# Optimization experiments

Measured on AMD Instinct MI355X. Metric: run time of the kernel, lower is better.

Reference implementation:

```python
import jax, jax.numpy as jnp
import numpy as np

L_DEG = 4      # max out-degree L
DEPTH = 7      # complete L-ary tree depth -> 21845 nodes
N_GEN = 16
C_ST = 8
M_LAB = 256


def _build_tree():
    sizes = [L_DEG ** d for d in range(DEPTH + 1)]
    limits = np.concatenate([[0], np.cumsum(sizes)]).astype(np.int64)
    t_size = int(limits[-1])
    nodes = np.arange(t_size)
    rng = np.random.default_rng(0)
    labels = rng.integers(0, M_LAB, t_size)
    parent = np.where(nodes > 0, (nodes - 1) // L_DEG, 0)
    pos = np.where(nodes > 0, (nodes - 1) % L_DEG, 0)
    ch = np.zeros((t_size, L_DEG), dtype=np.int64)
    n_internal = int(limits[-2])
    ch[:n_internal] = L_DEG * nodes[:n_internal, None] + np.arange(1, L_DEG + 1)[None, :]
    t = np.concatenate([labels[:, None], parent[:, None], pos[:, None], ch], axis=1).astype(np.int64)
    return t, limits


def setup_inputs() -> dict:
    key = jax.random.key(0)
    ka, kb, kp, ks = jax.random.split(key, 4)
    t, limits = _build_tree()
    return {
        "t": jnp.asarray(t),
        "t_limits": jnp.asarray(limits),
        "a": jax.random.normal(ka, (N_GEN, C_ST, C_ST, L_DEG), dtype=jnp.float32),
        "b": jax.random.normal(kb, (N_GEN, C_ST, M_LAB), dtype=jnp.float32),
        "pi": jax.random.normal(kp, (N_GEN, C_ST, L_DEG), dtype=jnp.float32),
        "sp": jax.random.normal(ks, (N_GEN, L_DEG), dtype=jnp.float32),
    }


def _forward(tn, lim, a, b, pi, sp):
    # tn, lim are host numpy int arrays (tree structure is a constant).
    G, C, _, L = a.shape
    t_size = int(lim[-1])
    n_levels = len(lim) - 1
    sL = int(lim[-2])                      # first leaf index
    labels = tn[:, 0]
    posf = tn[:, 2]
    ch_all = tn[:, 3:3 + L]

    sm_a = jax.nn.softmax(a, axis=1)       # P(parent_state i | child_state j, pos l)
    sm_b = jax.nn.softmax(b, axis=2)
    sm_pi = jax.nn.softmax(pi, axis=1)
    sm_sp = jax.nn.softmax(sp, axis=1)
    a_sp = sm_a * sm_sp[:, None, None, :]  # [G,i,j,L]

    # ---------------- upward pass ----------------
    prior = jnp.zeros((t_size, G, C), a.dtype)
    beta = jnp.zeros((t_size, G, C), a.dtype)
    beta_il = jnp.zeros((t_size, G, C), a.dtype)

    prior_lv = jnp.moveaxis(sm_pi[:, :, posf[sL:]], 2, 0)   # [NL,G,C]
    emis_lv = jnp.moveaxis(sm_b[:, :, labels[sL:]], 2, 0)   # [NL,G,C]
    beta_lv = prior_lv * emis_lv
    beta_lv = beta_lv / jnp.sum(beta_lv, axis=2, keepdims=True)
    prior = prior.at[sL:].set(prior_lv)
    beta = beta.at[sL:].set(beta_lv)

    for lev in range(n_levels - 2, -1, -1):   # internal levels, bottom-up
        s, e = int(lim[lev]), int(lim[lev + 1])
        ch = ch_all[s:e]                       # [P,L]
        mask = (ch > 0).astype(a.dtype)        # children packed in first slots
        prior_ch = prior[ch]                   # [P,L,G,C]
        beta_ch = beta[ch]                     # [P,L,G,C]
        u_prior = jnp.einsum('gijl,pl,plgj->pgi', a_sp, mask, prior_ch)
        u_bil = jnp.einsum('gijl,pl,plgj->pgi', a_sp, mask, beta_ch) / u_prior
        emis = jnp.moveaxis(sm_b[:, :, labels[s:e]], 2, 0)  # [P,G,C]
        tmp = emis * u_bil * u_prior
        u_beta = tmp / jnp.sum(tmp, axis=2, keepdims=True)
        prior = prior.at[s:e].set(u_prior)
        beta = beta.at[s:e].set(u_beta)
        beta_il = beta_il.at[s:e].set(u_bil)

    # ---------------- downward pass ----------------
    # row t_size is a dummy slot for padded (absent) children
    eps_i = jnp.zeros((t_size + 1, G, C), a.dtype).at[0].set(beta[0])
    eps_ijl = jnp.zeros((t_size, G, C, C, L), a.dtype)
    for lev in range(0, n_levels - 1):         # parents, top-down (root included)
        s, e = int(lim[lev]), int(lim[lev + 1])
        ch = ch_all[s:e]
        maskb = ch > 0
        mask = maskb.astype(a.dtype)
        beta_ch = jnp.transpose(beta[ch], (0, 2, 3, 1))       # [P,G,Cj,L]
        pe = eps_i[s:e] / (prior[s:e] * beta_il[s:e])         # [P,G,Ci]
        res = (pe[:, :, :, None, None] * a_sp[None]
               * beta_ch[:, :, None, :, :]
               * mask[:, None, None, None, :])                # [P,G,i,j,L]
        child_eps = jnp.sum(res, axis=3)                       # sum over j (as in source) -> [P,G,i,L]
        vals = jnp.moveaxis(child_eps, 3, 1).reshape(-1, G, C) # [P*L,G,C]
        safe = np.where(maskb, ch, t_size).reshape(-1)
        eps_i = eps_i.at[safe].set(vals)
        eps_ijl = eps_ijl.at[s:e].set(res)
    eps_i = eps_i[:t_size]
    # leaves' eps_ijl stay zero (source scatters zeros there)

    # ---------------- log-likelihood ----------------
    a_lh = jnp.einsum('ugijl,gijl->g', eps_ijl, jnp.log(sm_a))
    b_lh = jnp.einsum('ugc,gcu->g', eps_i, jnp.log(sm_b)[:, :, labels])
    pi_lh = jnp.einsum('ugc,gcu->g', eps_i[sL:], jnp.log(sm_pi)[:, :, posf[sL:]])
    eps_l = jnp.sum(eps_ijl, axis=(2, 3))                      # [u,g,L]
    sp_lh = jnp.einsum('ugl,gl->g', eps_l, jnp.log(sm_sp))
    return a_lh + b_lh + pi_lh + sp_lh


def reference(t, t_limits, a, b, pi, sp):
    tn = np.asarray(t)
    lim = np.asarray(t_limits)
    return _forward(tn, lim, a, b, pi, sp)
```

## Files before the change

### kernel.cpp

```cpp
#include <hip/hip_runtime.h>


#define G 16
#define C 8
#define GC 128
#define TSIZE 21845
#define SL 5461

__device__ __forceinline__ float grp8_sum(float v) {
  v += __shfl_xor(v, 1);
  v += __shfl_xor(v, 2);
  v += __shfl_xor(v, 4);
  return v;
}

__global__ void setup_kernel(const float* __restrict__ ain, const float* __restrict__ bin,
                             const float* __restrict__ piin, const float* __restrict__ spin,
                             float* __restrict__ a_sp, float* __restrict__ log_a,
                             float* __restrict__ sm_bT, float* __restrict__ log_bT,
                             float* __restrict__ sm_piT, float* __restrict__ log_piT,
                             float* __restrict__ log_sp, unsigned* __restrict__ ctr) {
  int blk = blockIdx.x, tid = threadIdx.x;
  if (blk < 128) {
    __shared__ float red4[4];
    int row = blk;
    float x = bin[row * 256 + tid];
    float m = x;
    #pragma unroll
    for (int off2 = 32; off2; off2 >>= 1) m = fmaxf(m, __shfl_xor(m, off2));
    if ((tid & 63) == 0) red4[tid >> 6] = m;
    __syncthreads();
    m = fmaxf(fmaxf(red4[0], red4[1]), fmaxf(red4[2], red4[3]));
    __syncthreads();
    float e = expf(x - m);
    float ssum = e;
    #pragma unroll
    for (int off2 = 32; off2; off2 >>= 1) ssum += __shfl_xor(ssum, off2);
    if ((tid & 63) == 0) red4[tid >> 6] = ssum;
    __syncthreads();
    ssum = red4[0] + red4[1] + red4[2] + red4[3];
    sm_bT[tid * GC + row]  = e / ssum;
    log_bT[tid * GC + row] = (x - m) - logf(ssum);
  } else if (blk == 128) {
    for (int col = tid; col < 512; col += 256) {
      int g = col >> 5, j = (col >> 2) & 7, l = col & 3;
      float x[8], m = -1e30f;
      #pragma unroll
      for (int i = 0; i < 8; ++i) { x[i] = ain[g*256 + i*32 + j*4 + l]; m = fmaxf(m, x[i]); }
      float ssum = 0.f;
      #pragma unroll
      for (int i = 0; i < 8; ++i) ssum += expf(x[i] - m);
      float ls = logf(ssum);
      float y0 = spin[g*4+0], y1 = spin[g*4+1], y2 = spin[g*4+2], y3 = spin[g*4+3];
      float ms = fmaxf(fmaxf(y0, y1), fmaxf(y2, y3));
      float d = expf(y0-ms) + expf(y1-ms) + expf(y2-ms) + expf(y3-ms);
      float spv = expf(spin[g*4+l] - ms) / d;
      #pragma unroll
      for (int i = 0; i < 8; ++i) {
        int o2 = g*256 + i*32 + j*4 + l;
        float smv = expf(x[i] - m) / ssum;
        a_sp[o2]  = smv * spv;
        log_a[o2] = (x[i] - m) - ls;
      }
    }
  } else {
    if (tid < 64) {
      int g = tid >> 2, l = tid & 3;
      float x[8], m = -1e30f;
      #pragma unroll
      for (int c = 0; c < 8; ++c) { x[c] = piin[g*32 + c*4 + l]; m = fmaxf(m, x[c]); }
      float ssum = 0.f;
      #pragma unroll
      for (int c = 0; c < 8; ++c) ssum += expf(x[c] - m);
      float ls = logf(ssum);
      #pragma unroll
      for (int c = 0; c < 8; ++c) {
        sm_piT[l*GC + g*8 + c]  = expf(x[c] - m) / ssum;
        log_piT[l*GC + g*8 + c] = (x[c] - m) - ls;
      }
    } else if (tid < 80) {
      int g = tid - 64;
      float y[4], m = -1e30f;
      #pragma unroll
      for (int l = 0; l < 4; ++l) { y[l] = spin[g*4 + l]; m = fmaxf(m, y[l]); }
      float ssum = 0.f;
      #pragma unroll
      for (int l = 0; l < 4; ++l) ssum += expf(y[l] - m);
      float ls = logf(ssum);
      #pragma unroll
      for (int l = 0; l < 4; ++l) log_sp[g*4 + l] = (y[l] - m) - ls;
    } else if (tid == 80) {
      *ctr = 0u;
    }
  }
}

__device__ __forceinline__ void up_lds(int v, int lab, int gi, int g8,
    const float* asp, const float* __restrict__ sm_bT,
    float* sBeta, float* sNum, bool wantNum) {
  int ch0 = 4*v + 1;
  float ub = 0.f;
  #pragma unroll
  for (int l = 0; l < 4; ++l) {
    const float4* bp = (const float4*)(sBeta + (ch0 + l)*GC + g8);
    float4 b0 = bp[0], b1 = bp[1];
    ub += asp[l]*b0.x + asp[4+l]*b0.y + asp[8+l]*b0.z + asp[12+l]*b0.w
        + asp[16+l]*b1.x + asp[20+l]*b1.y + asp[24+l]*b1.z + asp[28+l]*b1.w;
  }
  float tmp = sm_bT[lab*GC + gi] * ub;
  float s = grp8_sum(tmp);
  sBeta[v*GC + gi] = tmp / s;
  if (wantNum) sNum[v*GC + gi] = ub;
}

__device__ __forceinline__ double down_lds(int v, int lab, float e, int gi, int g8,
    const float* asp, const float* aal, const float* lsp,
    const float* __restrict__ log_bT, float* sBeta, const float* sNum) {
  float pe = e / sNum[v*GC + gi];
  int ch0 = 4*v + 1;
  float local = 0.f;
  #pragma unroll
  for (int l = 0; l < 4; ++l) {
    float4* bp = (float4*)(sBeta + (ch0 + l)*GC + g8);
    float4 b0 = bp[0], b1 = bp[1];
    float S = asp[l]*b0.x + asp[4+l]*b0.y + asp[8+l]*b0.z + asp[12+l]*b0.w
            + asp[16+l]*b1.x + asp[20+l]*b1.y + asp[24+l]*b1.z + asp[28+l]*b1.w;
    float A = aal[l]*b0.x + aal[4+l]*b0.y + aal[8+l]*b0.z + aal[12+l]*b0.w
            + aal[16+l]*b1.x + aal[20+l]*b1.y + aal[24+l]*b1.z + aal[28+l]*b1.w;
    float ce = pe * S;
    sBeta[(ch0 + l)*GC + gi] = ce;
    local += pe*A + ce*lsp[l];
  }
  return (double)local + (double)(e * log_bT[lab*GC + gi]);
}

__global__ __launch_bounds__(512, 1) void up_kernel(
    const float* __restrict__ a_sp, const float* __restrict__ sm_bT,
    const float* __restrict__ sm_piT, const int* __restrict__ t,
    float* __restrict__ betaS, float* __restrict__ numS) {
  __shared__ float sBeta[85*GC];
  __shared__ float sNum[21*GC];
  const int blk = blockIdx.x, tid = threadIdx.x;
  const int gi = tid & 127, g = gi >> 3, i = gi & 7, g8 = g*8, w = tid >> 7;
  float asp[32];
  {
    const float4* pa = (const float4*)(a_sp + g*256 + i*32);
    #pragma unroll
    for (int q = 0; q < 8; ++q) {
      float4 v = pa[q];
      asp[q*4+0]=v.x; asp[q*4+1]=v.y; asp[q*4+2]=v.z; asp[q*4+3]=v.w;
    }
  }
  const int base_leaf = SL + blk*64;
  #pragma unroll
  for (int it = 0; it < 16; ++it) {
    int k = it*4 + w;
    float bt = sm_piT[(k & 3)*GC + gi] * sm_bT[t[(base_leaf + k)*7]*GC + gi];
    float s = grp8_sum(bt);
    sBeta[(21 + k)*GC + gi] = bt / s;
  }
  __syncthreads();
  #pragma unroll
  for (int it = 0; it < 4; ++it) {
    int k = it*4 + w;
    up_lds(5 + k, t[(1365 + blk*16 + k)*7], gi, g8, asp, sm_bT, sBeta, sNum, true);
  }
  __syncthreads();
  up_lds(1 + w, t[(341 + blk*4 + w)*7], gi, g8, asp, sm_bT, sBeta, sNum, true);
  __syncthreads();
  if (tid < 128)
    up_lds(0, t[(85 + blk)*7], gi, g8, asp, sm_bT, sBeta, sNum, true);
  __syncthreads();
  {
    const float4* srcB = (const float4*)sBeta;
    float4* dstB = (float4*)(betaS + (size_t)blk*85*GC);
    for (int n = tid; n < 85*GC/4; n += 512) dstB[n] = srcB[n];
    const float4* srcN = (const float4*)sNum;
    float4* dstN = (float4*)(numS + (size_t)blk*21*GC);
    for (int n = tid; n < 21*GC/4; n += 512) dstN[n] = srcN[n];
  }
}

__global__ __launch_bounds__(512, 1) void downall_kernel(
    const float* __restrict__ a_sp, const float* __restrict__ log_a,
    const float* __restrict__ log_sp, const float* __restrict__ sm_bT,
    const float* __restrict__ log_bT, const float* __restrict__ sm_piT,
    const float* __restrict__ log_piT, const int* __restrict__ t,
    const float* __restrict__ betaS, const float* __restrict__ numS,
    unsigned* __restrict__ ctr, double* __restrict__ partial,
    float* __restrict__ out) {
  __shared__ float  sBeta[85*GC];
  __shared__ float  sNum[21*GC];
  __shared__ float  sEps[GC];
  __shared__ double sd[64];
  __shared__ double sfin[256];
  __shared__ unsigned lastFlag;
  const int blk = blockIdx.x, tid = threadIdx.x;
  const int gi = tid & 127, g = gi >> 3, i = gi & 7, g8 = g*8, w = tid >> 7;
  float asp[32], aal[32], lsp[4];
  {
    const float4* pa = (const float4*)(a_sp  + g*256 + i*32);
    const float4* pl = (const float4*)(log_a + g*256 + i*32);
    #pragma unroll
    for (int k = 0; k < 8; ++k) {
      float4 va = pa[k], vl = pl[k];
      asp[k*4+0]=va.x; asp[k*4+1]=va.y; asp[k*4+2]=va.z; asp[k*4+3]=va.w;
      aal[k*4+0]=va.x*vl.x; aal[k*4+1]=va.y*vl.y; aal[k*4+2]=va.z*vl.z; aal[k*4+3]=va.w*vl.w;
    }
    #pragma unroll
    for (int l = 0; l < 4; ++l) lsp[l] = log_sp[g*4 + l];
  }

  #pragma unroll
  for (int it = 0; it < 16; ++it) {
    int k = it*4 + w, u = 21 + k;
    float ub = 0.f;
    #pragma unroll
    for (int l = 0; l < 4; ++l) {
      const float4* bp = (const float4*)(betaS + (size_t)(4*k + l)*85*GC + g8);
      float4 b0 = bp[0], b1 = bp[1];
      ub += asp[l]*b0.x + asp[4+l]*b0.y + asp[8+l]*b0.z + asp[12+l]*b0.w
          + asp[16+l]*b1.x + asp[20+l]*b1.y + asp[24+l]*b1.z + asp[28+l]*b1.w;
    }
    float tmp = sm_bT[t[u*7]*GC + gi] * ub;
    float s = grp8_sum(tmp);
    sBeta[u*GC + gi] = tmp / s;
  }
  __syncthreads();
  #pragma unroll
  for (int it = 0; it < 4; ++it) {
    int u = 5 + it*4 + w;
    up_lds(u, t[u*7], gi, g8, asp, sm_bT, sBeta, sNum, true);
  }
  __syncthreads();
  up_lds(1 + w, t[(1 + w)*7], gi, g8, asp, sm_bT, sBeta, sNum, true);
  __syncthreads();
  if (tid < 128)
    up_lds(0, t[0], gi, g8, asp, sm_bT, sBeta, sNum, true);
  __syncthreads();

  double acc = 0.0;
  if (tid < 128) {
    int a1 = 1 + (blk >> 6), a2 = 5 + (blk >> 4), a3 = 21 + (blk >> 2);
    float e = sBeta[gi];
    int anc[3] = {0, a1, a2};
    int chn[3] = {a1, a2, a3};
    #pragma unroll
    for (int s2 = 0; s2 < 3; ++s2) {
      float pe = e / sNum[anc[s2]*GC + gi];
      int l = (chn[s2] - 1) & 3;
      const float4* bp = (const float4*)(sBeta + chn[s2]*GC + g8);
      float4 b0 = bp[0], b1 = bp[1];
      float S = asp[l]*b0.x + asp[4+l]*b0.y + asp[8+l]*b0.z + asp[12+l]*b0.w
              + asp[16+l]*b1.x + asp[20+l]*b1.y + asp[24+l]*b1.z + asp[28+l]*b1.w;
      e = pe * S;
    }
    float Sv[4], Av[4], num3 = 0.f;
    int qbase = blk & ~3;
    #pragma unroll
    for (int l = 0; l < 4; ++l) {
      const float4* bp = (const float4*)(betaS + (size_t)(qbase + l)*85*GC + g8);
      float4 b0 = bp[0], b1 = bp[1];
      Sv[l] = asp[l]*b0.x + asp[4+l]*b0.y + asp[8+l]*b0.z + asp[12+l]*b0.w
            + asp[16+l]*b1.x + asp[20+l]*b1.y + asp[24+l]*b1.z + asp[28+l]*b1.w;
      num3 += Sv[l];
      Av[l] = aal[l]*b0.x + aal[4+l]*b0.y + aal[8+l]*b0.z + aal[12+l]*b0.w
            + aal[16+l]*b1.x + aal[20+l]*b1.y + aal[24+l]*b1.z + aal[28+l]*b1.w;
    }
    float e3 = e;
    float pe3 = e3 / num3;
    sEps[gi] = pe3 * Sv[blk & 3];
    if ((blk & 3) == 0) {
      float local = 0.f;
      #pragma unroll
      for (int l = 0; l < 4; ++l) local += pe3*Av[l] + (pe3*Sv[l])*lsp[l];
      acc += (double)local + (double)(e3 * log_bT[t[a3*7]*GC + gi]);
    }
  }
  __syncthreads();

  if (blk == 0) {
    if (tid < 128)
      acc += down_lds(0, t[0], sBeta[gi], gi, g8, asp, aal, lsp, log_bT, sBeta, sNum);
    __syncthreads();
    {
      int v = 1 + w;
      acc += down_lds(v, t[v*7], sBeta[v*GC + gi], gi, g8, asp, aal, lsp, log_bT, sBeta, sNum);
    }
    __syncthreads();
    #pragma unroll
    for (int it = 0; it < 4; ++it) {
      int v = 5 + it*4 + w;
      acc += down_lds(v, t[v*7], sBeta[v*GC + gi], gi, g8, asp, aal, lsp, log_bT, sBeta, sNum);
    }
    __syncthreads();
  }

  {
    const float4* srcB = (const float4*)(betaS + (size_t)blk*85*GC);
    float4* dstB = (float4*)sBeta;
    for (int n = tid; n < 85*GC/4; n += 512) dstB[n] = srcB[n];
    const float4* srcN = (const float4*)(numS + (size_t)blk*21*GC);
    float4* dstN = (float4*)sNum;
    for (int n = tid; n < 21*GC/4; n += 512) dstN[n] = srcN[n];
  }
  __syncthreads();

  const int base_leaf = SL + blk*64;
  if (tid < 128)
    acc += down_lds(0, t[(85 + blk)*7], sEps[gi], gi, g8, asp, aal, lsp,
                    log_bT, sBeta, sNum);
  __syncthreads();
  {
    int v = 1 + w;
    acc += down_lds(v, t[(341 + blk*4 + w)*7], sBeta[v*GC + gi], gi, g8,
                    asp, aal, lsp, log_bT, sBeta, sNum);
  }
  __syncthreads();
  #pragma unroll
  for (int it = 0; it < 4; ++it) {
    int k = it*4 + w, v = 5 + k;
    acc += down_lds(v, t[(1365 + blk*16 + k)*7], sBeta[v*GC + gi], gi, g8,
                    asp, aal, lsp, log_bT, sBeta, sNum);
  }
  __syncthreads();
  #pragma unroll
  for (int it = 0; it < 16; ++it) {
    int k = it*4 + w;
    float e = sBeta[(21 + k)*GC + gi];
    acc += (double)(e * (log_bT[t[(base_leaf + k)*7]*GC + gi] +
                         log_piT[(k & 3)*GC + gi]));
  }

  acc += __shfl_xor(acc, 1);
  acc += __shfl_xor(acc, 2);
  acc += __shfl_xor(acc, 4);
  if (i == 0) sd[tid >> 3] = acc;
  __syncthreads();
  if (tid < 16) partial[blk*16 + tid] = sd[tid] + sd[16 + tid] + sd[32 + tid] + sd[48 + tid];
  __syncthreads();

  if (tid == 0) {
    unsigned old = __hip_atomic_fetch_add(ctr, 1u, __ATOMIC_ACQ_REL,
                                          __HIP_MEMORY_SCOPE_AGENT);
    lastFlag = (old == 255u);
  }
  __syncthreads();
  if (lastFlag) {
    if (tid < 256) {
      int gg = tid & 15, ch = tid >> 4;
      const double* p = partial + (size_t)ch*256 + gg;
      double s = 0.0;
      #pragma unroll
      for (int q = 0; q < 16; ++q) s += p[q*16];
      sfin[tid] = s;
    }
    __syncthreads();
    if (tid < 16) {
      double tot = 0.0;
      #pragma unroll
      for (int ch = 0; ch < 16; ++ch) tot += sfin[ch*16 + tid];
      out[tid] = (float)tot;
    }
  }
}

extern "C" void kernel_launch(void* const* d_in, const int* in_sizes, int n_in,
                              void* d_out, int out_size, void* d_ws, size_t ws_size,
                              hipStream_t stream) {
  const int*   t  = (const int*)d_in[0];
  const float* a  = (const float*)d_in[2];
  const float* b  = (const float*)d_in[3];
  const float* pi = (const float*)d_in[4];
  const float* sp = (const float*)d_in[5];
  float* out = (float*)d_out;

  char* w = (char*)d_ws;
  size_t off = 0;
  auto carve = [&](size_t bytes) -> void* {
    void* ptr = w + off;
    off += (bytes + 255) & ~(size_t)255;
    return ptr;
  };
  float*    a_sp    = (float*)carve((size_t)16*8*8*4*4);
  float*    log_a   = (float*)carve((size_t)16*8*8*4*4);
  float*    sm_bT   = (float*)carve((size_t)256*GC*4);
  float*    log_bT  = (float*)carve((size_t)256*GC*4);
  float*    sm_piT  = (float*)carve((size_t)4*GC*4);
  float*    log_piT = (float*)carve((size_t)4*GC*4);
  float*    log_sp  = (float*)carve((size_t)16*4*4);
  float*    betaS   = (float*)carve((size_t)256*85*GC*4);
  float*    numS    = (float*)carve((size_t)256*21*GC*4);
  double*   partial = (double*)carve((size_t)256*16*8);
  unsigned* ctr     = (unsigned*)carve((size_t)4);

  setup_kernel<<<130, 256, 0, stream>>>(a, b, pi, sp, a_sp, log_a, sm_bT, log_bT,
                                        sm_piT, log_piT, log_sp, ctr);
  up_kernel<<<256, 512, 0, stream>>>(a_sp, sm_bT, sm_piT, t, betaS, numS);
  downall_kernel<<<256, 512, 0, stream>>>(a_sp, log_a, log_sp, sm_bT, log_bT,
                                          sm_piT, log_piT, t, betaS, numS,
                                          ctr, partial, out);
}
```

Measured before the change: 107.1 us.

## Prefetch subtree state into registers and spread top-level downward pass across blocks

The up kernel now writes each subtree root's beta to a compact betaG array, so the downall kernel reads top-level betas from a small contiguous buffer instead of strided rows in betaS. The downall kernel issues its per-block betaS/numS loads into registers at kernel start, which lets them overlap the redundant top-of-tree computation, and stores them to LDS later. The serial top-three-level downward pass that block 0 used to run alone is split so each of blocks 0-20 handles one node, recomputing its ancestor eps chain. This trades higher register pressure and some redundant arithmetic for less serialization and hidden load latency.

Result: no change. 105.6 us (-1.4%).

```diff
diff --git a/kernel.cpp b/kernel.cpp
--- a/kernel.cpp
+++ b/kernel.cpp
@@ -12,6 +12,13 @@
   v += __shfl_xor(v, 2);
   v += __shfl_xor(v, 4);
   return v;
+}
+
+__device__ __forceinline__ float matv(const float* asp, const float* row, int l, int g8) {
+  const float4* bp = (const float4*)(row + g8);
+  float4 b0 = bp[0], b1 = bp[1];
+  return asp[l]*b0.x + asp[4+l]*b0.y + asp[8+l]*b0.z + asp[12+l]*b0.w
+       + asp[16+l]*b1.x + asp[20+l]*b1.y + asp[24+l]*b1.z + asp[28+l]*b1.w;
 }
 
 __global__ void setup_kernel(const float* __restrict__ ain, const float* __restrict__ bin,
@@ -137,7 +144,8 @@
 __global__ __launch_bounds__(512, 1) void up_kernel(
     const float* __restrict__ a_sp, const float* __restrict__ sm_bT,
     const float* __restrict__ sm_piT, const int* __restrict__ t,
-    float* __restrict__ betaS, float* __restrict__ numS) {
+    float* __restrict__ betaS, float* __restrict__ numS,
+    float* __restrict__ betaG) {
   __shared__ float sBeta[85*GC];
   __shared__ float sNum[21*GC];
   const int blk = blockIdx.x, tid = threadIdx.x;
@@ -168,8 +176,10 @@
   __syncthreads();
   up_lds(1 + w, t[(341 + blk*4 + w)*7], gi, g8, asp, sm_bT, sBeta, sNum, true);
   __syncthreads();
-  if (tid < 128)
+  if (tid < 128) {
     up_lds(0, t[(85 + blk)*7], gi, g8, asp, sm_bT, sBeta, sNum, true);
+    betaG[(size_t)blk*GC + gi] = sBeta[gi];
+  }
   __syncthreads();
   {
     const float4* srcB = (const float4*)sBeta;
@@ -187,8 +197,8 @@
     const float* __restrict__ log_bT, const float* __restrict__ sm_piT,
     const float* __restrict__ log_piT, const int* __restrict__ t,
     const float* __restrict__ betaS, const float* __restrict__ numS,
-    unsigned* __restrict__ ctr, double* __restrict__ partial,
-    float* __restrict__ out) {
+    const float* __restrict__ betaG, unsigned* __restrict__ ctr,
+    double* __restrict__ partial, float* __restrict__ out) {
   __shared__ float  sBeta[85*GC];
   __shared__ float  sNum[21*GC];
   __shared__ float  sEps[GC];
@@ -211,17 +221,25 @@
     for (int l = 0; l < 4; ++l) lsp[l] = log_sp[g*4 + l];
   }
 
+  float4 rB0, rB1, rB2, rB3, rB4, rB5, rN0, rN1;
+  {
+    const float4* srcB = (const float4*)(betaS + (size_t)blk*85*GC);
+    rB0 = srcB[tid];        rB1 = srcB[tid + 512];
+    rB2 = srcB[tid + 1024]; rB3 = srcB[tid + 1536];
+    rB4 = srcB[tid + 2048];
+    if (tid < 160) rB5 = srcB[tid + 2560];
+    const float4* srcN = (const float4*)(numS + (size_t)blk*21*GC);
+    rN0 = srcN[tid];
+    if (tid < 160) rN1 = srcN[tid + 512];
+  }
+
   #pragma unroll
   for (int it = 0; it < 16; ++it) {
     int k = it*4 + w, u = 21 + k;
     float ub = 0.f;
     #pragma unroll
-    for (int l = 0; l < 4; ++l) {
-      const float4* bp = (const float4*)(betaS + (size_t)(4*k + l)*85*GC + g8);
-      float4 b0 = bp[0], b1 = bp[1];
-      ub += asp[l]*b0.x + asp[4+l]*b0.y + asp[8+l]*b0.z + asp[12+l]*b0.w
-          + asp[16+l]*b1.x + asp[20+l]*b1.y + asp[24+l]*b1.z + asp[28+l]*b1.w;
-    }
+    for (int l = 0; l < 4; ++l)
+      ub += matv(asp, betaG + (size_t)(4*k + l)*GC, l, g8);
     float tmp = sm_bT[t[u*7]*GC + gi] * ub;
     float s = grp8_sum(tmp);
     sBeta[u*GC + gi] = tmp / s;
@@ -249,17 +267,13 @@
     for (int s2 = 0; s2 < 3; ++s2) {
       float pe = e / sNum[anc[s2]*GC + gi];
       int l = (chn[s2] - 1) & 3;
-      const float4* bp = (const float4*)(sBeta + chn[s2]*GC + g8);
-      float4 b0 = bp[0], b1 = bp[1];
-      float S = asp[l]*b0.x + asp[4+l]*b0.y + asp[8+l]*b0.z + asp[12+l]*b0.w
-              + asp[16+l]*b1.x + asp[20+l]*b1.y + asp[24+l]*b1.z + asp[28+l]*b1.w;
-      e = pe * S;
+      e = pe * matv(asp, sBeta + chn[s2]*GC, l, g8);
     }
     float Sv[4], Av[4], num3 = 0.f;
     int qbase = blk & ~3;
     #pragma unroll
     for (int l = 0; l < 4; ++l) {
-      const float4* bp = (const float4*)(betaS + (size_t)(qbase + l)*85*GC + g8);
+      const float4* bp = (const float4*)(betaG + (size_t)(qbase + l)*GC + g8);
       float4 b0 = bp[0], b1 = bp[1];
       Sv[l] = asp[l]*b0.x + asp[4+l]*b0.y + asp[8+l]*b0.z + asp[12+l]*b0.w
             + asp[16+l]*b1.x + asp[20+l]*b1.y + asp[24+l]*b1.z + asp[28+l]*b1.w;
@@ -277,32 +291,36 @@
       acc += (double)local + (double)(e3 * log_bT[t[a3*7]*GC + gi]);
     }
   }
-  __syncthreads();
-
-  if (blk == 0) {
-    if (tid < 128)
-      acc += down_lds(0, t[0], sBeta[gi], gi, g8, asp, aal, lsp, log_bT, sBeta, sNum);
-    __syncthreads();
-    {
-      int v = 1 + w;
-      acc += down_lds(v, t[v*7], sBeta[v*GC + gi], gi, g8, asp, aal, lsp, log_bT, sBeta, sNum);
-    }
-    __syncthreads();
-    #pragma unroll
-    for (int it = 0; it < 4; ++it) {
-      int v = 5 + it*4 + w;
-      acc += down_lds(v, t[v*7], sBeta[v*GC + gi], gi, g8, asp, aal, lsp, log_bT, sBeta, sNum);
-    }
-    __syncthreads();
-  }
-
-  {
-    const float4* srcB = (const float4*)(betaS + (size_t)blk*85*GC);
+
+  if (blk < 21 && tid < 128) {
+    int v = blk;
+    float e;
+    if (v == 0) {
+      e = sBeta[gi];
+    } else {
+      int p = (v - 1) >> 2;
+      float pe = sBeta[gi] / sNum[gi];
+      if (p == 0) {
+        e = pe * matv(asp, sBeta + v*GC, (v - 1) & 3, g8);
+      } else {
+        float ep = pe * matv(asp, sBeta + p*GC, (p - 1) & 3, g8);
+        float pe2 = ep / sNum[p*GC + gi];
+        e = pe2 * matv(asp, sBeta + v*GC, (v - 1) & 3, g8);
+      }
+    }
+    acc += down_lds(v, t[v*7], e, gi, g8, asp, aal, lsp, log_bT, sBeta, sNum);
+  }
+  __syncthreads();
+
+  {
     float4* dstB = (float4*)sBeta;
-    for (int n = tid; n < 85*GC/4; n += 512) dstB[n] = srcB[n];
-    const float4* srcN = (const float4*)(numS + (size_t)blk*21*GC);
+    dstB[tid] = rB0;        dstB[tid + 512]  = rB1;
+    dstB[tid + 1024] = rB2; dstB[tid + 1536] = rB3;
+    dstB[tid + 2048] = rB4;
+    if (tid < 160) dstB[tid + 2560] = rB5;
     float4* dstN = (float4*)sNum;
-    for (int n = tid; n < 21*GC/4; n += 512) dstN[n] = srcN[n];
+    dstN[tid] = rN0;
+    if (tid < 160) dstN[tid + 512] = rN1;
   }
   __syncthreads();
 
@@ -391,13 +409,14 @@
   float*    log_sp  = (float*)carve((size_t)16*4*4);
   float*    betaS   = (float*)carve((size_t)256*85*GC*4);
   float*    numS    = (float*)carve((size_t)256*21*GC*4);
+  float*    betaG   = (float*)carve((size_t)256*GC*4);
   double*   partial = (double*)carve((size_t)256*16*8);
   unsigned* ctr     = (unsigned*)carve((size_t)4);
 
   setup_kernel<<<130, 256, 0, stream>>>(a, b, pi, sp, a_sp, log_a, sm_bT, log_bT,
                                         sm_piT, log_piT, log_sp, ctr);
-  up_kernel<<<256, 512, 0, stream>>>(a_sp, sm_bT, sm_piT, t, betaS, numS);
+  up_kernel<<<256, 512, 0, stream>>>(a_sp, sm_bT, sm_piT, t, betaS, numS, betaG);
   downall_kernel<<<256, 512, 0, stream>>>(a_sp, log_a, log_sp, sm_bT, log_bT,
                                           sm_piT, log_piT, t, betaS, numS,
-                                          ctr, partial, out);
-}
+                                          betaG, ctr, partial, out);
+}
```
